# Kernel tuning notes

Measured on AMD Instinct MI355X. Metric: run time of the kernel, lower is better.

The kernel has to match this reference:

```python
import jax, jax.numpy as jnp
import numpy as np

DIM = 2048
N_HEADS = 16
HEAD_DIM = DIM // N_HEADS  # 128
KV_RANK = 512
MAX_SEQ = 2048
EPS = 1e-6


def _precompute_freqs(dim, end, theta=10000.0):
    freqs = 1.0 / theta ** (np.arange(0, dim, 2)[: dim // 2].astype(np.float32) / dim)
    t = np.arange(end, dtype=np.float32)
    ang = np.outer(t, freqs)  # [end, dim//2]
    return jnp.asarray(np.cos(ang)), jnp.asarray(np.sin(ang))


def setup_inputs() -> dict:
    key = jax.random.key(0)
    ks = jax.random.split(key, 6)
    s = 0.02
    x = jax.random.normal(ks[0], (1, 2048, DIM), dtype=jnp.float32)
    wq = jax.random.normal(ks[1], (N_HEADS * HEAD_DIM, DIM), dtype=jnp.float32) * s
    w_kv_down = jax.random.normal(ks[2], (KV_RANK, DIM), dtype=jnp.float32) * s
    w_kv_up = jax.random.normal(ks[3], (2 * N_HEADS * HEAD_DIM, KV_RANK), dtype=jnp.float32) * s
    wo = jax.random.normal(ks[4], (DIM, N_HEADS * HEAD_DIM), dtype=jnp.float32) * s
    q_norm_w = jnp.ones((HEAD_DIM,), dtype=jnp.float32)
    k_norm_w = jnp.ones((HEAD_DIM,), dtype=jnp.float32)
    freqs_cos, freqs_sin = _precompute_freqs(HEAD_DIM, MAX_SEQ)
    return {"x": x, "wq": wq, "w_kv_down": w_kv_down, "w_kv_up": w_kv_up,
            "wo": wo, "q_norm_w": q_norm_w, "k_norm_w": k_norm_w,
            "freqs_cos": freqs_cos, "freqs_sin": freqs_sin}


def _rmsnorm(x, w):
    var = jnp.mean(x * x, axis=-1, keepdims=True)
    return x * jax.lax.rsqrt(var + EPS) * w


def _rope(x, cos, sin):
    # x: [B,T,H,D] -> pairs [B,T,H,D/2,2]; cos/sin: [T,D/2] broadcast over heads
    xr = x.reshape(*x.shape[:-1], -1, 2)
    re, im = xr[..., 0], xr[..., 1]
    c = cos[None, :, None, :]
    s = sin[None, :, None, :]
    out = jnp.stack([re * c - im * s, re * s + im * c], axis=-1)
    return out.reshape(x.shape)


def reference(x, wq, w_kv_down, w_kv_up, wo, q_norm_w, k_norm_w, freqs_cos, freqs_sin):
    B, T, C = x.shape
    H, D = N_HEADS, HEAD_DIM
    xq = jnp.einsum('btc,ec->bte', x, wq).reshape(B, T, H, D)
    latent = jnp.einsum('btc,rc->btr', x, w_kv_down)            # [B,T,R]
    kv = jnp.einsum('btr,er->bte', latent, w_kv_up).reshape(B, T, 2, H, D)
    xk, xv = kv[:, :, 0], kv[:, :, 1]
    xq = _rmsnorm(xq, q_norm_w)
    xk = _rmsnorm(xk, k_norm_w)
    cos, sin = freqs_cos[:T], freqs_sin[:T]
    xq = _rope(xq, cos, sin)
    xk = _rope(xk, cos, sin)
    scale = 1.0 / jnp.sqrt(jnp.asarray(D, dtype=x.dtype))
    scores = jnp.einsum('bthd,bshd->bhts', xq, xk) * scale       # [B,H,T,T]
    causal = jnp.tril(jnp.ones((T, T), dtype=bool))
    scores = jnp.where(causal, scores, jnp.finfo(scores.dtype).min)
    attn = jax.nn.softmax(scores, axis=-1)
    out = jnp.einsum('bhts,bshd->bthd', attn, xv).reshape(B, T, C)
    return jnp.einsum('bte,ce->btc', out, wo)
```

## Files before the change

kernel.cpp:

```cpp
#include <hip/hip_runtime.h>

#define T_SEQ 2048
#define DIM   2048
#define NH    16
#define HD    128
#define KVR   512

typedef unsigned short ushort_t;
typedef __attribute__((ext_vector_type(8))) short   short8;
typedef __attribute__((ext_vector_type(8))) __bf16  bf16x8;
typedef __attribute__((ext_vector_type(4))) float   f32x4;
typedef __attribute__((ext_vector_type(4))) unsigned int u32x4;

union V8 { short8 s; bf16x8 b; u32x4 u; };

__device__ inline float b2f(ushort_t u) {
    union { unsigned u; float f; } x; x.u = ((unsigned)u) << 16; return x.f;
}
__device__ inline ushort_t f2b(float f) {
    union { float f; unsigned u; } x; x.f = f;
    unsigned r = x.u + 0x7FFFu + ((x.u >> 16) & 1u);
    return (ushort_t)(r >> 16);
}

__device__ __forceinline__ void gld16(char* lds, const ushort_t* g) {
    __builtin_amdgcn_global_load_lds(
        (const __attribute__((address_space(1))) unsigned int*)g,
        (__attribute__((address_space(3))) unsigned int*)lds,
        16, 0, 0);
}

__global__ __launch_bounds__(256) void cvtk(
    const float* __restrict__ a0, const float* __restrict__ a1,
    const float* __restrict__ a2, const float* __restrict__ a3,
    const float* __restrict__ a4,
    ushort_t* __restrict__ b0, ushort_t* __restrict__ b1,
    ushort_t* __restrict__ b2, ushort_t* __restrict__ b3,
    ushort_t* __restrict__ b4)
{
    const int N0 = 524288, N1 = 1048576, N2 = 1179648, N3 = 1441792, N4 = 1966080;
    for (int c = blockIdx.x * blockDim.x + threadIdx.x; c < N4; c += gridDim.x * blockDim.x) {
        const float* s; ushort_t* d; int off;
        if      (c < N0) { s = a0; d = b0; off = c; }
        else if (c < N1) { s = a1; d = b1; off = c - N0; }
        else if (c < N2) { s = a2; d = b2; off = c - N1; }
        else if (c < N3) { s = a3; d = b3; off = c - N2; }
        else             { s = a4; d = b4; off = c - N3; }
        f32x4 lo = *(const f32x4*)(s + (size_t)off * 8);
        f32x4 hi = *(const f32x4*)(s + (size_t)off * 8 + 4);
        V8 v;
        #pragma unroll
        for (int e = 0; e < 4; ++e) { v.b[e] = (__bf16)lo[e]; v.b[e + 4] = (__bf16)hi[e]; }
        *(u32x4*)(d + (size_t)off * 8) = v.u;
    }
}

template <int BM, int BN, bool OUT_F32, bool NORM>
__global__ __launch_bounds__(256, 2) void gemm_nt(
    const ushort_t* __restrict__ A, const ushort_t* __restrict__ B,
    void* __restrict__ Cv, int M, int K,
    const ushort_t* __restrict__ B2, void* __restrict__ C2, int Nsplit, int N2,
    const float* __restrict__ NW, const float* __restrict__ FC,
    const float* __restrict__ FS, int normLimit)
{
    constexpr int GM = BM / 64;
    constexpr int WN = BN * GM / 4;
    constexpr int NJ = WN / 16;
    constexpr int AR = BM / 32;
    constexpr int BR = BN / 32;

    __shared__ __align__(16) char sA[2][BM * 128];
    __shared__ __align__(16) char sB[2][BN * 128];

    const int tid  = threadIdx.x;
    const int wave = tid >> 6;
    const int lane = tid & 63;
    const int l15  = lane & 15;
    const int l4   = lane >> 4;

    const int gridX = gridDim.x;
    int idlin = blockIdx.y * gridX + blockIdx.x;
    const int cpx = (gridX * gridDim.y) >> 3;
    idlin = (idlin & 7) * cpx + (idlin >> 3);
    const int bm = (idlin % gridX) * BM;
    const int bn = (idlin / gridX) * BN;

    const ushort_t* Bp = B;
    void* Cp = Cv; int ldC = Nsplit; int bnl = bn;
    if (B2 != nullptr && bn >= Nsplit) { Bp = B2; Cp = C2; ldC = N2; bnl = bn - Nsplit; }

    const int wmo = (GM == 2) ? (wave >> 1) * 64 : 0;
    const int wno = (GM == 2) ? (wave & 1) * WN : wave * WN;

    const int lp   = lane ^ ((lane >> 3) & 7);
    const int prow = lp >> 3;
    const int psub = lp & 7;
    const ushort_t* aSrc[AR];
    const ushort_t* bSrc[BR];
    #pragma unroll
    for (int i = 0; i < AR; ++i) {
        int r = wave * (BM / 4) + i * 8 + prow;
        aSrc[i] = A + (size_t)(bm + r) * K + psub * 8;
    }
    #pragma unroll
    for (int i = 0; i < BR; ++i) {
        int r = wave * (BN / 4) + i * 8 + prow;
        bSrc[i] = Bp + (size_t)(bnl + r) * K + psub * 8;
    }
    const int ldsOffA = wave * (BM * 32);
    const int ldsOffB = wave * (BN * 32);

    f32x4 acc[4][NJ] = {};
    const int nk = K >> 6;

    #pragma unroll
    for (int i = 0; i < AR; ++i) gld16(&sA[0][ldsOffA + i * 1024], aSrc[i]);
    #pragma unroll
    for (int i = 0; i < BR; ++i) gld16(&sB[0][ldsOffB + i * 1024], bSrc[i]);

    int cur = 0;
    for (int k = 0; k < nk; ++k) {
        __syncthreads();
        if (k + 1 < nk) {
            const int ko = (k + 1) * 64;
            #pragma unroll
            for (int i = 0; i < AR; ++i) gld16(&sA[cur ^ 1][ldsOffA + i * 1024], aSrc[i] + ko);
            #pragma unroll
            for (int i = 0; i < BR; ++i) gld16(&sB[cur ^ 1][ldsOffB + i * 1024], bSrc[i] + ko);
        }
        #pragma unroll
        for (int kk = 0; kk < 2; ++kk) {
            V8 a[4], b[NJ];
            #pragma unroll
            for (int i2 = 0; i2 < 4; ++i2) {
                int row = wmo + i2 * 16 + l15;
                a[i2].u = *(const u32x4*)(sA[cur] + ((row * 128 + kk * 64 + l4 * 16) ^ ((row & 7) << 4)));
            }
            #pragma unroll
            for (int j = 0; j < NJ; ++j) {
                int col = wno + j * 16 + l15;
                b[j].u = *(const u32x4*)(sB[cur] + ((col * 128 + kk * 64 + l4 * 16) ^ ((col & 7) << 4)));
            }
            #pragma unroll
            for (int i2 = 0; i2 < 4; ++i2)
                #pragma unroll
                for (int j = 0; j < NJ; ++j)
                    acc[i2][j] = __builtin_amdgcn_mfma_f32_16x16x32_bf16(a[i2].b, b[j].b, acc[i2][j], 0, 0, 0);
        }
        cur ^= 1;
    }

    const bool doNorm = NORM && (bn < normLimit);
    if (doNorm) {
        __syncthreads();
        float* sums = (float*)sA;
        #pragma unroll
        for (int i = 0; i < 4; ++i)
            #pragma unroll
            for (int r = 0; r < 4; ++r) {
                float ss = 0.f;
                #pragma unroll
                for (int j = 0; j < NJ; ++j) ss += acc[i][j][r] * acc[i][j][r];
                ss += __shfl_xor(ss, 1);
                ss += __shfl_xor(ss, 2);
                ss += __shfl_xor(ss, 4);
                ss += __shfl_xor(ss, 8);
                if (l15 == 0) sums[wave * 64 + i * 16 + l4 * 4 + r] = ss;
            }
        __syncthreads();
        #pragma unroll
        for (int i = 0; i < 4; ++i)
            #pragma unroll
            for (int r = 0; r < 4; ++r) {
                const int rloc = i * 16 + l4 * 4 + r;
                float tot;
                if constexpr (GM == 2) {
                    const int wb = wave & 2;
                    tot = sums[wb * 64 + rloc] + sums[(wb + 1) * 64 + rloc];
                } else {
                    tot = sums[rloc] + sums[64 + rloc] + sums[128 + rloc] + sums[192 + rloc];
                }
                const float inv = rsqrtf(tot * (1.0f / 128.0f) + 1e-6f);
                const int t = bm + wmo + rloc;
                #pragma unroll
                for (int j = 0; j < NJ; ++j) {
                    const int col = wno + j * 16 + l15;
                    float v = acc[i][j][r] * inv * NW[col];
                    float partner = __shfl_xor(v, 1);
                    const float c = FC[(size_t)t * 64 + (col >> 1)];
                    const float s = FS[(size_t)t * 64 + (col >> 1)];
                    float outv = (l15 & 1) ? (partner * s + v * c)
                                           : (v * c - partner * s);
                    ((ushort_t*)Cp)[(size_t)t * ldC + bnl + col] = f2b(outv);
                }
            }
        return;
    }

    #pragma unroll
    for (int i = 0; i < 4; ++i)
        #pragma unroll
        for (int j = 0; j < NJ; ++j)
            #pragma unroll
            for (int r = 0; r < 4; ++r) {
                int rowg = bm + wmo + i * 16 + l4 * 4 + r;
                int colg = bnl + wno + j * 16 + l15;
                if constexpr (OUT_F32)
                    ((float*)Cp)[(size_t)rowg * ldC + colg] = acc[i][j][r];
                else
                    ((ushort_t*)Cp)[(size_t)rowg * ldC + colg] = f2b(acc[i][j][r]);
            }
}

#define STAGE_LOAD(kv0) do { \
  _Pragma("unroll") for (int rr = 0; rr < 4; ++rr) \
    kreg[rr] = *(const u32x4*)(KV + (size_t)((kv0) + krow[rr]) * (2 * DIM) + h * HD + kc8 * 8); \
  _Pragma("unroll") for (int rr = 0; rr < 2; ++rr) \
    _Pragma("unroll") for (int e = 0; e < 8; ++e) \
      vreg[rr][e] = *(const unsigned*)(KV + (size_t)((kv0) + vkvb[rr] * 8 + e) * (2 * DIM) + DIM + h * HD + vd); \
} while (0)

#define STAGE_WRITE(sKb, sVb) do { \
  _Pragma("unroll") for (int rr = 0; rr < 4; ++rr) \
    *(u32x4*)((sKb) + ((krow[rr] * 256 + kc8 * 16) ^ ((krow[rr] & 7) << 4))) = kreg[rr]; \
  _Pragma("unroll") for (int rr = 0; rr < 2; ++rr) { \
    V8 lo, hi; \
    _Pragma("unroll") for (int e = 0; e < 8; ++e) { \
      lo.s[e] = (short)(vreg[rr][e] & 0xFFFFu); hi.s[e] = (short)(vreg[rr][e] >> 16); } \
    *(u32x4*)((sVb) + ((vd * 128 + vkvb[rr] * 16) ^ ((vd & 7) << 4)))             = lo.u; \
    *(u32x4*)((sVb) + (((vd + 1) * 128 + vkvb[rr] * 16) ^ (((vd + 1) & 7) << 4))) = hi.u; \
  } \
} while (0)

__global__ __launch_bounds__(512) void attn_kernel(
    const ushort_t* __restrict__ Q,
    const ushort_t* __restrict__ KV,
    ushort_t* __restrict__ O)
{
    __shared__ __align__(16) char sAll[131072];

    const int id    = blockIdx.x;
    const int xcd   = id & 7;
    const int slot  = id >> 3;
    const int h     = xcd * 2 + (slot >> 4);
    const int pairb = slot & 15;

    const int tid   = threadIdx.x;
    const int gid   = tid >> 8;
    const int wtid  = tid & 255;
    const int wave4 = wtid >> 6;
    const int lane  = tid & 63;
    const int Qq    = lane & 15;
    const int G     = lane >> 4;

    char* gbase = sAll + gid * 65536;

    const int krow[4] = { (0*256 + wtid) >> 4, (1*256 + wtid) >> 4,
                          (2*256 + wtid) >> 4, (3*256 + wtid) >> 4 };
    const int kc8 = wtid & 15;
    const int vd  = lane * 2;
    const int vkvb[2] = { wave4, 4 + wave4 };

    const float scale2 = 0.08838834764831845f * 1.4426950408889634f;
    const float M2     = 20.0f;

    u32x4 kreg[4];
    unsigned vreg[2][8];

    #pragma unroll
    for (int phase = 0; phase < 2; ++phase) {
        const int jt  = phase ? (31 - pairb) : pairb;
        const int q0w = jt * 64 + wave4 * 16;

        V8 qf[4];
        #pragma unroll
        for (int kk = 0; kk < 4; ++kk)
            qf[kk].u = *(const u32x4*)(Q + (size_t)(q0w + Qq) * DIM + h * HD + kk * 32 + G * 8);

        f32x4 o[8] = {};
        float lrow = 0.f;

        const int n_g = (jt >= gid) ? ((jt - gid) >> 1) + 1 : 0;
        const int nA  = (jt >> 1) + 1;

        if (n_g > 0) {
            STAGE_LOAD(gid * 64);
            STAGE_WRITE(gbase, gbase + 32768);
        }

        int cur = 0;
        for (int s = 0; s < nA; ++s) {
            __syncthreads();

            const bool pf = (s + 1 < n_g);
            if (pf) STAGE_LOAD((2 * (s + 1) + gid) * 64);

            if (s < n_g) {
                const int tcur = 2 * s + gid;
                const int kv0  = tcur * 64;
                char* sKb = gbase + cur * 16384;
                char* sVb = gbase + 32768 + cur * 16384;

                f32x4 sacc[4] = {};
                __builtin_amdgcn_s_setprio(1);
                #pragma unroll
                for (int kk = 0; kk < 4; ++kk) {
                    #pragma unroll
                    for (int cb = 0; cb < 4; ++cb) {
                        int row = cb * 16 + Qq;
                        V8 kf;
                        kf.u = *(const u32x4*)(sKb + ((row * 256 + kk * 64 + G * 16) ^ ((row & 7) << 4)));
                        sacc[cb] = __builtin_amdgcn_mfma_f32_16x16x32_bf16(kf.b, qf[kk].b, sacc[cb], 0, 0, 0);
                    }
                }
                __builtin_amdgcn_s_setprio(0);

                float p[4][4];
                float rs = 0.f;
                const int qg = q0w + Qq;
                #pragma unroll
                for (int cb = 0; cb < 4; ++cb)
                    #pragma unroll
                    for (int r = 0; r < 4; ++r) {
                        float s2 = sacc[cb][r] * scale2 - M2;
                        if (tcur == jt) {
                            int kvg = kv0 + cb * 16 + G * 4 + r;
                            if (kvg > qg) s2 = -1e30f;
                        }
                        float e = exp2f(s2);
                        p[cb][r] = e;
                        rs += e;
                    }
                rs += __shfl_xor(rs, 16);
                rs += __shfl_xor(rs, 32);
                lrow += rs;

                unsigned pk[4][2];
                #pragma unroll
                for (int cb = 0; cb < 4; ++cb) {
                    pk[cb][0] = (unsigned)f2b(p[cb][0]) | ((unsigned)f2b(p[cb][1]) << 16);
                    pk[cb][1] = (unsigned)f2b(p[cb][2]) | ((unsigned)f2b(p[cb][3]) << 16);
                }

                const int sLo = ((G & 1) * 2) * 16 + Qq;
                const int sHi = sLo + 16;
                const bool hiC = (G >> 1);
                #pragma unroll
                for (int kk2 = 0; kk2 < 2; ++kk2) {
                    const int c0 = kk2 * 2, c1 = c0 + 1;
                    unsigned w0a = __shfl(pk[c0][0], sLo), w0b = __shfl(pk[c1][0], sLo);
                    unsigned w1a = __shfl(pk[c0][1], sLo), w1b = __shfl(pk[c1][1], sLo);
                    unsigned w2a = __shfl(pk[c0][0], sHi), w2b = __shfl(pk[c1][0], sHi);
                    unsigned w3a = __shfl(pk[c0][1], sHi), w3b = __shfl(pk[c1][1], sHi);
                    V8 pa;
                    pa.u[0] = hiC ? w0b : w0a;
                    pa.u[1] = hiC ? w1b : w1a;
                    pa.u[2] = hiC ? w2b : w2a;
                    pa.u[3] = hiC ? w3b : w3a;
                    __builtin_amdgcn_s_setprio(1);
                    #pragma unroll
                    for (int nb = 0; nb < 8; ++nb) {
                        int d = nb * 16 + Qq;
                        V8 vf;
                        vf.u = *(const u32x4*)(sVb + ((d * 128 + kk2 * 64 + G * 16) ^ ((d & 7) << 4)));
                        o[nb] = __builtin_amdgcn_mfma_f32_16x16x32_bf16(pa.b, vf.b, o[nb], 0, 0, 0);
                    }
                    __builtin_amdgcn_s_setprio(0);
                }
            }

            if (pf) STAGE_WRITE(gbase + (cur ^ 1) * 16384, gbase + 32768 + (cur ^ 1) * 16384);
            cur ^= 1;
        }

        __syncthreads();
        float* mrg = (float*)sAll;
        float* mlb = (float*)(sAll + 33792);
        if (gid == 1) {
            #pragma unroll
            for (int nb = 0; nb < 8; ++nb)
                #pragma unroll
                for (int r = 0; r < 4; ++r) {
                    int qloc = wave4 * 16 + G * 4 + r;
                    mrg[qloc * 132 + nb * 16 + Qq] = o[nb][r];
                }
            if (G == 0) {
                int qloc = wave4 * 16 + Qq;
                mlb[qloc] = lrow;
            }
        }
        __syncthreads();
        if (gid == 0) {
            int qloc0 = wave4 * 16 + Qq;
            float lB = mlb[qloc0];
            float linv = 1.f / (lrow + lB);
            float lir[4];
            #pragma unroll
            for (int r = 0; r < 4; ++r)
                lir[r] = __shfl(linv, G * 4 + r);
            #pragma unroll
            for (int nb = 0; nb < 8; ++nb)
                #pragma unroll
                for (int r = 0; r < 4; ++r) {
                    int qloc = wave4 * 16 + G * 4 + r;
                    float ob  = mrg[qloc * 132 + nb * 16 + Qq];
                    float val = (o[nb][r] + ob) * lir[r];
                    int qgr = jt * 64 + qloc;
                    O[(size_t)qgr * DIM + h * HD + nb * 16 + Qq] = f2b(val);
                }
        }
        __syncthreads();
    }
}

extern "C" void kernel_launch(void* const* d_in, const int* in_sizes, int n_in,
                              void* d_out, int out_size, void* d_ws, size_t ws_size,
                              hipStream_t stream)
{
    const float* x    = (const float*)d_in[0];
    const float* wq   = (const float*)d_in[1];
    const float* wkvd = (const float*)d_in[2];
    const float* wkvu = (const float*)d_in[3];
    const float* wo   = (const float*)d_in[4];
    const float* qnw  = (const float*)d_in[5];
    const float* knw  = (const float*)d_in[6];
    const float* fc   = (const float*)d_in[7];
    const float* fs   = (const float*)d_in[8];
    float* out = (float*)d_out;

    char* ws = (char*)d_ws;
    const size_t MB = 1024 * 1024;
    ushort_t* xb    = (ushort_t*)(ws);
    ushort_t* att   = (ushort_t*)(ws);
    ushort_t* Qb    = (ushort_t*)(ws + 8  * MB);
    ushort_t* wqb   = (ushort_t*)(ws + 16 * MB);
    ushort_t* wkvdb = (ushort_t*)(ws + 24 * MB);
    ushort_t* kvb   = (ushort_t*)(ws + 16 * MB);
    ushort_t* lat   = (ushort_t*)(ws + 32 * MB);
    ushort_t* wkvub = (ushort_t*)(ws + 34 * MB);
    ushort_t* wob   = (ushort_t*)(ws + 38 * MB);

    cvtk<<<dim3(2048), dim3(256), 0, stream>>>(x, wq, wkvd, wkvu, wo,
                                               xb, wqb, wkvdb, wkvub, wob);
    gemm_nt<64, 128, false, true><<<dim3(32, 20), dim3(256), 0, stream>>>(
        xb, wqb, Qb, 2048, 2048, wkvdb, lat, 2048, 512, qnw, fc, fs, 2048);
    gemm_nt<128, 128, false, true><<<dim3(16, 32), dim3(256), 0, stream>>>(
        lat, wkvub, kvb, 2048, 512, nullptr, nullptr, 4096, 0, knw, fc, fs, 2048);
    attn_kernel<<<dim3(256), dim3(512), 0, stream>>>(Qb, kvb, att);
    gemm_nt<128, 64, true, false><<<dim3(16, 32), dim3(256), 0, stream>>>(
        att, wob, out, 2048, 2048, nullptr, nullptr, 2048, 0, nullptr, nullptr, nullptr, 0);
}
```

Before: 159.1 us.

## Load K tiles directly to LDS via global-load-to-LDS and reswizzle V layout

K tiles are now copied straight from global memory into shared memory with a gld16 direct-to-LDS load, replacing the old path that staged them through registers. The swizzle is applied on the global column side so reads keep the existing XOR pattern. The V tile swizzle also changes to mix in higher row bits, to reduce LDS bank conflicts on the transposed V writes and reads. This frees registers and VALU work during prefetch, but the async LDS writes now depend on the existing barriers for ordering.

```diff
diff --git a/kernel.cpp b/kernel.cpp
--- a/kernel.cpp
+++ b/kernel.cpp
@@ -212,23 +212,29 @@
             }
 }
 
-#define STAGE_LOAD(kv0) do { \
-  _Pragma("unroll") for (int rr = 0; rr < 4; ++rr) \
-    kreg[rr] = *(const u32x4*)(KV + (size_t)((kv0) + krow[rr]) * (2 * DIM) + h * HD + kc8 * 8); \
+#define VSWZ(d) (((((d) & 7) ^ (((d) >> 3) & 7))) << 4)
+
+#define STAGE_LOAD_V(kv0) do { \
   _Pragma("unroll") for (int rr = 0; rr < 2; ++rr) \
     _Pragma("unroll") for (int e = 0; e < 8; ++e) \
       vreg[rr][e] = *(const unsigned*)(KV + (size_t)((kv0) + vkvb[rr] * 8 + e) * (2 * DIM) + DIM + h * HD + vd); \
 } while (0)
 
-#define STAGE_WRITE(sKb, sVb) do { \
-  _Pragma("unroll") for (int rr = 0; rr < 4; ++rr) \
-    *(u32x4*)((sKb) + ((krow[rr] * 256 + kc8 * 16) ^ ((krow[rr] & 7) << 4))) = kreg[rr]; \
+#define STAGE_WRITE_V(sVb) do { \
   _Pragma("unroll") for (int rr = 0; rr < 2; ++rr) { \
     V8 lo, hi; \
     _Pragma("unroll") for (int e = 0; e < 8; ++e) { \
       lo.s[e] = (short)(vreg[rr][e] & 0xFFFFu); hi.s[e] = (short)(vreg[rr][e] >> 16); } \
-    *(u32x4*)((sVb) + ((vd * 128 + vkvb[rr] * 16) ^ ((vd & 7) << 4)))             = lo.u; \
-    *(u32x4*)((sVb) + (((vd + 1) * 128 + vkvb[rr] * 16) ^ (((vd + 1) & 7) << 4))) = hi.u; \
+    *(u32x4*)((sVb) + ((vd * 128 + vkvb[rr] * 16) ^ VSWZ(vd)))             = lo.u; \
+    *(u32x4*)((sVb) + (((vd + 1) * 128 + vkvb[rr] * 16) ^ VSWZ(vd + 1))) = hi.u; \
+  } \
+} while (0)
+
+#define STAGE_K_GLD(sKb, kv0) do { \
+  _Pragma("unroll") for (int rr = 0; rr < 4; ++rr) { \
+    const int rowr = rr * 16 + (wtid >> 4); \
+    gld16((sKb) + rr * 4096 + wavegrp * 1024, \
+          KV + (size_t)((kv0) + rowr) * (2 * DIM) + h * HD + (kc8 ^ (rowr & 7)) * 8); \
   } \
 } while (0)
 
@@ -252,11 +258,10 @@
     const int lane  = tid & 63;
     const int Qq    = lane & 15;
     const int G     = lane >> 4;
+    const int wavegrp = wtid >> 6;
 
     char* gbase = sAll + gid * 65536;
 
-    const int krow[4] = { (0*256 + wtid) >> 4, (1*256 + wtid) >> 4,
-                          (2*256 + wtid) >> 4, (3*256 + wtid) >> 4 };
     const int kc8 = wtid & 15;
     const int vd  = lane * 2;
     const int vkvb[2] = { wave4, 4 + wave4 };
@@ -264,7 +269,6 @@
     const float scale2 = 0.08838834764831845f * 1.4426950408889634f;
     const float M2     = 20.0f;
 
-    u32x4 kreg[4];
     unsigned vreg[2][8];
 
     #pragma unroll
@@ -284,8 +288,9 @@
         const int nA  = (jt >> 1) + 1;
 
         if (n_g > 0) {
-            STAGE_LOAD(gid * 64);
-            STAGE_WRITE(gbase, gbase + 32768);
+            STAGE_K_GLD(gbase, gid * 64);
+            STAGE_LOAD_V(gid * 64);
+            STAGE_WRITE_V(gbase + 32768);
         }
 
         int cur = 0;
@@ -293,7 +298,10 @@
             __syncthreads();
 
             const bool pf = (s + 1 < n_g);
-            if (pf) STAGE_LOAD((2 * (s + 1) + gid) * 64);
+            if (pf) {
+                STAGE_K_GLD(gbase + (cur ^ 1) * 16384, (2 * (s + 1) + gid) * 64);
+                STAGE_LOAD_V((2 * (s + 1) + gid) * 64);
+            }
 
             if (s < n_g) {
                 const int tcur = 2 * s + gid;
@@ -362,14 +370,14 @@
                     for (int nb = 0; nb < 8; ++nb) {
                         int d = nb * 16 + Qq;
                         V8 vf;
-                        vf.u = *(const u32x4*)(sVb + ((d * 128 + kk2 * 64 + G * 16) ^ ((d & 7) << 4)));
+                        vf.u = *(const u32x4*)(sVb + ((d * 128 + kk2 * 64 + G * 16) ^ VSWZ(d)));
                         o[nb] = __builtin_amdgcn_mfma_f32_16x16x32_bf16(pa.b, vf.b, o[nb], 0, 0, 0);
                     }
                     __builtin_amdgcn_s_setprio(0);
                 }
             }
 
-            if (pf) STAGE_WRITE(gbase + (cur ^ 1) * 16384, gbase + 32768 + (cur ^ 1) * 16384);
+            if (pf) STAGE_WRITE_V(gbase + 32768 + (cur ^ 1) * 16384);
             cur ^= 1;
         }
 
```

After: 156.3 us (median of 2 runs). No clear change (-1.8%).

## Split attention blocks per query tile, halve LDS and single-buffer K/V

Applied to the files above, without the earlier changes.

The attention kernel no longer pairs a short and a long causal query tile per block. It launches one block per (head, query tile) with the longest tiles scheduled first, which doubles the grid. Shared memory drops from 128KB to 64KB by single-buffering K/V, with register prefetch and an extra barrier per iteration, so more blocks can be resident per CU. The V tile swizzle now also XORs in the higher row bits to reduce LDS bank conflicts. The cost is less overlap of LDS writes with compute, and heavier-first ordering is relied on to balance load.

```diff
diff --git a/kernel.cpp b/kernel.cpp
--- a/kernel.cpp
+++ b/kernel.cpp
@@ -212,6 +212,8 @@
             }
 }
 
+#define VSWZ(d) (((((d) & 7) ^ (((d) >> 3) & 7))) << 4)
+
 #define STAGE_LOAD(kv0) do { \
   _Pragma("unroll") for (int rr = 0; rr < 4; ++rr) \
     kreg[rr] = *(const u32x4*)(KV + (size_t)((kv0) + krow[rr]) * (2 * DIM) + h * HD + kc8 * 8); \
@@ -227,8 +229,8 @@
     V8 lo, hi; \
     _Pragma("unroll") for (int e = 0; e < 8; ++e) { \
       lo.s[e] = (short)(vreg[rr][e] & 0xFFFFu); hi.s[e] = (short)(vreg[rr][e] >> 16); } \
-    *(u32x4*)((sVb) + ((vd * 128 + vkvb[rr] * 16) ^ ((vd & 7) << 4)))             = lo.u; \
-    *(u32x4*)((sVb) + (((vd + 1) * 128 + vkvb[rr] * 16) ^ (((vd + 1) & 7) << 4))) = hi.u; \
+    *(u32x4*)((sVb) + ((vd * 128 + vkvb[rr] * 16) ^ VSWZ(vd)))           = lo.u; \
+    *(u32x4*)((sVb) + (((vd + 1) * 128 + vkvb[rr] * 16) ^ VSWZ(vd + 1))) = hi.u; \
   } \
 } while (0)
 
@@ -237,13 +239,13 @@
     const ushort_t* __restrict__ KV,
     ushort_t* __restrict__ O)
 {
-    __shared__ __align__(16) char sAll[131072];
-
-    const int id    = blockIdx.x;
-    const int xcd   = id & 7;
-    const int slot  = id >> 3;
-    const int h     = xcd * 2 + (slot >> 4);
-    const int pairb = slot & 15;
+    __shared__ __align__(16) char sAll[65536];
+
+    const int id  = blockIdx.x;
+    const int xcd = id & 7;
+    const int s_  = id >> 3;
+    const int h   = xcd * 2 + (s_ & 1);
+    const int jt  = 31 - (s_ >> 1);
 
     const int tid   = threadIdx.x;
     const int gid   = tid >> 8;
@@ -253,7 +255,8 @@
     const int Qq    = lane & 15;
     const int G     = lane >> 4;
 
-    char* gbase = sAll + gid * 65536;
+    char* sK = sAll + gid * 32768;
+    char* sV = sAll + gid * 32768 + 16384;
 
     const int krow[4] = { (0*256 + wtid) >> 4, (1*256 + wtid) >> 4,
                           (2*256 + wtid) >> 4, (3*256 + wtid) >> 4 };
@@ -267,149 +270,135 @@
     u32x4 kreg[4];
     unsigned vreg[2][8];
 
-    #pragma unroll
-    for (int phase = 0; phase < 2; ++phase) {
-        const int jt  = phase ? (31 - pairb) : pairb;
-        const int q0w = jt * 64 + wave4 * 16;
-
-        V8 qf[4];
-        #pragma unroll
-        for (int kk = 0; kk < 4; ++kk)
-            qf[kk].u = *(const u32x4*)(Q + (size_t)(q0w + Qq) * DIM + h * HD + kk * 32 + G * 8);
-
-        f32x4 o[8] = {};
-        float lrow = 0.f;
-
-        const int n_g = (jt >= gid) ? ((jt - gid) >> 1) + 1 : 0;
-        const int nA  = (jt >> 1) + 1;
-
-        if (n_g > 0) {
-            STAGE_LOAD(gid * 64);
-            STAGE_WRITE(gbase, gbase + 32768);
-        }
-
-        int cur = 0;
-        for (int s = 0; s < nA; ++s) {
-            __syncthreads();
-
-            const bool pf = (s + 1 < n_g);
-            if (pf) STAGE_LOAD((2 * (s + 1) + gid) * 64);
-
-            if (s < n_g) {
-                const int tcur = 2 * s + gid;
-                const int kv0  = tcur * 64;
-                char* sKb = gbase + cur * 16384;
-                char* sVb = gbase + 32768 + cur * 16384;
-
-                f32x4 sacc[4] = {};
+    const int q0w = jt * 64 + wave4 * 16;
+
+    V8 qf[4];
+    #pragma unroll
+    for (int kk = 0; kk < 4; ++kk)
+        qf[kk].u = *(const u32x4*)(Q + (size_t)(q0w + Qq) * DIM + h * HD + kk * 32 + G * 8);
+
+    f32x4 o[8] = {};
+    float lrow = 0.f;
+
+    const int n_g = (jt >= gid) ? ((jt - gid) >> 1) + 1 : 0;
+    const int nA  = (jt >> 1) + 1;
+
+    if (n_g > 0) STAGE_LOAD(gid * 64);
+
+    for (int s = 0; s < nA; ++s) {
+        __syncthreads();
+        if (s < n_g) STAGE_WRITE(sK, sV);
+        __syncthreads();
+        if (s + 1 < n_g) STAGE_LOAD((2 * (s + 1) + gid) * 64);
+
+        if (s < n_g) {
+            const int tcur = 2 * s + gid;
+            const int kv0  = tcur * 64;
+
+            f32x4 sacc[4] = {};
+            __builtin_amdgcn_s_setprio(1);
+            #pragma unroll
+            for (int kk = 0; kk < 4; ++kk) {
+                #pragma unroll
+                for (int cb = 0; cb < 4; ++cb) {
+                    int row = cb * 16 + Qq;
+                    V8 kf;
+                    kf.u = *(const u32x4*)(sK + ((row * 256 + kk * 64 + G * 16) ^ ((row & 7) << 4)));
+                    sacc[cb] = __builtin_amdgcn_mfma_f32_16x16x32_bf16(kf.b, qf[kk].b, sacc[cb], 0, 0, 0);
+                }
+            }
+            __builtin_amdgcn_s_setprio(0);
+
+            float p[4][4];
+            float rs = 0.f;
+            const int qg = q0w + Qq;
+            #pragma unroll
+            for (int cb = 0; cb < 4; ++cb)
+                #pragma unroll
+                for (int r = 0; r < 4; ++r) {
+                    float s2 = sacc[cb][r] * scale2 - M2;
+                    if (tcur == jt) {
+                        int kvg = kv0 + cb * 16 + G * 4 + r;
+                        if (kvg > qg) s2 = -1e30f;
+                    }
+                    float e = exp2f(s2);
+                    p[cb][r] = e;
+                    rs += e;
+                }
+            rs += __shfl_xor(rs, 16);
+            rs += __shfl_xor(rs, 32);
+            lrow += rs;
+
+            unsigned pk[4][2];
+            #pragma unroll
+            for (int cb = 0; cb < 4; ++cb) {
+                pk[cb][0] = (unsigned)f2b(p[cb][0]) | ((unsigned)f2b(p[cb][1]) << 16);
+                pk[cb][1] = (unsigned)f2b(p[cb][2]) | ((unsigned)f2b(p[cb][3]) << 16);
+            }
+
+            const int sLo = ((G & 1) * 2) * 16 + Qq;
+            const int sHi = sLo + 16;
+            const bool hiC = (G >> 1);
+            #pragma unroll
+            for (int kk2 = 0; kk2 < 2; ++kk2) {
+                const int c0 = kk2 * 2, c1 = c0 + 1;
+                unsigned w0a = __shfl(pk[c0][0], sLo), w0b = __shfl(pk[c1][0], sLo);
+                unsigned w1a = __shfl(pk[c0][1], sLo), w1b = __shfl(pk[c1][1], sLo);
+                unsigned w2a = __shfl(pk[c0][0], sHi), w2b = __shfl(pk[c1][0], sHi);
+                unsigned w3a = __shfl(pk[c0][1], sHi), w3b = __shfl(pk[c1][1], sHi);
+                V8 pa;
+                pa.u[0] = hiC ? w0b : w0a;
+                pa.u[1] = hiC ? w1b : w1a;
+                pa.u[2] = hiC ? w2b : w2a;
+                pa.u[3] = hiC ? w3b : w3a;
                 __builtin_amdgcn_s_setprio(1);
                 #pragma unroll
-                for (int kk = 0; kk < 4; ++kk) {
-                    #pragma unroll
-                    for (int cb = 0; cb < 4; ++cb) {
-                        int row = cb * 16 + Qq;
-                        V8 kf;
-                        kf.u = *(const u32x4*)(sKb + ((row * 256 + kk * 64 + G * 16) ^ ((row & 7) << 4)));
-                        sacc[cb] = __builtin_amdgcn_mfma_f32_16x16x32_bf16(kf.b, qf[kk].b, sacc[cb], 0, 0, 0);
-                    }
+                for (int nb = 0; nb < 8; ++nb) {
+                    int d = nb * 16 + Qq;
+                    V8 vf;
+                    vf.u = *(const u32x4*)(sV + ((d * 128 + kk2 * 64 + G * 16) ^ VSWZ(d)));
+                    o[nb] = __builtin_amdgcn_mfma_f32_16x16x32_bf16(pa.b, vf.b, o[nb], 0, 0, 0);
                 }
                 __builtin_amdgcn_s_setprio(0);
-
-                float p[4][4];
-                float rs = 0.f;
-                const int qg = q0w + Qq;
-                #pragma unroll
-                for (int cb = 0; cb < 4; ++cb)
-                    #pragma unroll
-                    for (int r = 0; r < 4; ++r) {
-                        float s2 = sacc[cb][r] * scale2 - M2;
-                        if (tcur == jt) {
-                            int kvg = kv0 + cb * 16 + G * 4 + r;
-                            if (kvg > qg) s2 = -1e30f;
-                        }
-                        float e = exp2f(s2);
-                        p[cb][r] = e;
-                        rs += e;
-                    }
-                rs += __shfl_xor(rs, 16);
-                rs += __shfl_xor(rs, 32);
-                lrow += rs;
-
-                unsigned pk[4][2];
-                #pragma unroll
-                for (int cb = 0; cb < 4; ++cb) {
-                    pk[cb][0] = (unsigned)f2b(p[cb][0]) | ((unsigned)f2b(p[cb][1]) << 16);
-                    pk[cb][1] = (unsigned)f2b(p[cb][2]) | ((unsigned)f2b(p[cb][3]) << 16);
-                }
-
-                const int sLo = ((G & 1) * 2) * 16 + Qq;
-                const int sHi = sLo + 16;
-                const bool hiC = (G >> 1);
-                #pragma unroll
-                for (int kk2 = 0; kk2 < 2; ++kk2) {
-                    const int c0 = kk2 * 2, c1 = c0 + 1;
-                    unsigned w0a = __shfl(pk[c0][0], sLo), w0b = __shfl(pk[c1][0], sLo);
-                    unsigned w1a = __shfl(pk[c0][1], sLo), w1b = __shfl(pk[c1][1], sLo);
-                    unsigned w2a = __shfl(pk[c0][0], sHi), w2b = __shfl(pk[c1][0], sHi);
-                    unsigned w3a = __shfl(pk[c0][1], sHi), w3b = __shfl(pk[c1][1], sHi);
-                    V8 pa;
-                    pa.u[0] = hiC ? w0b : w0a;
-                    pa.u[1] = hiC ? w1b : w1a;
-                    pa.u[2] = hiC ? w2b : w2a;
-                    pa.u[3] = hiC ? w3b : w3a;
-                    __builtin_amdgcn_s_setprio(1);
-                    #pragma unroll
-                    for (int nb = 0; nb < 8; ++nb) {
-                        int d = nb * 16 + Qq;
-                        V8 vf;
-                        vf.u = *(const u32x4*)(sVb + ((d * 128 + kk2 * 64 + G * 16) ^ ((d & 7) << 4)));
-                        o[nb] = __builtin_amdgcn_mfma_f32_16x16x32_bf16(pa.b, vf.b, o[nb], 0, 0, 0);
-                    }
-                    __builtin_amdgcn_s_setprio(0);
-                }
-            }
-
-            if (pf) STAGE_WRITE(gbase + (cur ^ 1) * 16384, gbase + 32768 + (cur ^ 1) * 16384);
-            cur ^= 1;
+            }
         }
-
-        __syncthreads();
-        float* mrg = (float*)sAll;
-        float* mlb = (float*)(sAll + 33792);
-        if (gid == 1) {
-            #pragma unroll
-            for (int nb = 0; nb < 8; ++nb)
-                #pragma unroll
-                for (int r = 0; r < 4; ++r) {
-                    int qloc = wave4 * 16 + G * 4 + r;
-                    mrg[qloc * 132 + nb * 16 + Qq] = o[nb][r];
-                }
-            if (G == 0) {
-                int qloc = wave4 * 16 + Qq;
-                mlb[qloc] = lrow;
-            }
+    }
+
+    __syncthreads();
+    float* mrg = (float*)sAll;
+    float* mlb = (float*)(sAll + 33792);
+    if (gid == 1) {
+        #pragma unroll
+        for (int nb = 0; nb < 8; ++nb)
+            #pragma unroll
+            for (int r = 0; r < 4; ++r) {
+                int qloc = wave4 * 16 + G * 4 + r;
+                mrg[qloc * 132 + nb * 16 + Qq] = o[nb][r];
+            }
+        if (G == 0) {
+            int qloc = wave4 * 16 + Qq;
+            mlb[qloc] = lrow;
         }
-        __syncthreads();
-        if (gid == 0) {
-            int qloc0 = wave4 * 16 + Qq;
-            float lB = mlb[qloc0];
-            float linv = 1.f / (lrow + lB);
-            float lir[4];
-            #pragma unroll
-            for (int r = 0; r < 4; ++r)
-                lir[r] = __shfl(linv, G * 4 + r);
-            #pragma unroll
-            for (int nb = 0; nb < 8; ++nb)
-                #pragma unroll
-                for (int r = 0; r < 4; ++r) {
-                    int qloc = wave4 * 16 + G * 4 + r;
-                    float ob  = mrg[qloc * 132 + nb * 16 + Qq];
-                    float val = (o[nb][r] + ob) * lir[r];
-                    int qgr = jt * 64 + qloc;
-                    O[(size_t)qgr * DIM + h * HD + nb * 16 + Qq] = f2b(val);
-                }
-        }
-        __syncthreads();
+    }
+    __syncthreads();
+    if (gid == 0) {
+        int qloc0 = wave4 * 16 + Qq;
+        float lB = mlb[qloc0];
+        float linv = 1.f / (lrow + lB);
+        float lir[4];
+        #pragma unroll
+        for (int r = 0; r < 4; ++r)
+            lir[r] = __shfl(linv, G * 4 + r);
+        #pragma unroll
+        for (int nb = 0; nb < 8; ++nb)
+            #pragma unroll
+            for (int r = 0; r < 4; ++r) {
+                int qloc = wave4 * 16 + G * 4 + r;
+                float ob  = mrg[qloc * 132 + nb * 16 + Qq];
+                float val = (o[nb][r] + ob) * lir[r];
+                int qgr = jt * 64 + qloc;
+                O[(size_t)qgr * DIM + h * HD + nb * 16 + Qq] = f2b(val);
+            }
     }
 }
 
@@ -446,7 +435,7 @@
         xb, wqb, Qb, 2048, 2048, wkvdb, lat, 2048, 512, qnw, fc, fs, 2048);
     gemm_nt<128, 128, false, true><<<dim3(16, 32), dim3(256), 0, stream>>>(
         lat, wkvub, kvb, 2048, 512, nullptr, nullptr, 4096, 0, knw, fc, fs, 2048);
-    attn_kernel<<<dim3(256), dim3(512), 0, stream>>>(Qb, kvb, att);
+    attn_kernel<<<dim3(512), dim3(512), 0, stream>>>(Qb, kvb, att);
     gemm_nt<128, 64, true, false><<<dim3(16, 32), dim3(256), 0, stream>>>(
         att, wob, out, 2048, 2048, nullptr, nullptr, 2048, 0, nullptr, nullptr, nullptr, 0);
 }
```

Measured after the change: 164.9 us. 1.04x slower.
